# Kernel tuning notes

Hardware: AMD Instinct MI355X
Metric: run time of the kernel (lower is better)

Reference implementation:

```python
import jax, jax.numpy as jnp
import numpy as np

N_VERTICES = 24  # hardcoded via torch.eye(24) in the original
K = 3


def normalized_adj(adj):
    # scipy version: L = (A @ D^-1/2).T @ D^-1/2 = D^-1/2 @ A^T @ D^-1/2
    d = adj.sum(axis=1)
    d_inv_sqrt = jnp.where(d > 0, 1.0 / jnp.sqrt(d), 0.0)
    return (adj * d_inv_sqrt[None, :]).T * d_inv_sqrt[None, :]


def cheb_polynomials(L, k_order):
    Ts = [jnp.eye(N_VERTICES, dtype=L.dtype), L]
    for _ in range(2, k_order):
        Ts.append(2.0 * L @ Ts[-1] - Ts[-2])
    return jnp.stack(Ts[:k_order])  # (K, N, N)


def setup_inputs() -> dict:
    key = jax.random.key(0)
    k1, k2, k3 = jax.random.split(key, 3)
    x = jax.random.normal(k1, (64, 32, N_VERTICES, 512), dtype=jnp.float32)
    adj = jax.random.uniform(k2, (N_VERTICES, N_VERTICES), dtype=jnp.float32)
    Theta = jax.random.normal(k3, (K, 32, 32), dtype=jnp.float32)
    return {"x": x, "adj": adj, "Theta": Theta}


def reference(x, adj, Theta):
    # x: (b, c, n, t); adj: (n, n); Theta: (K, c, o)
    L = normalized_adj(adj)
    T = cheb_polynomials(L, K)  # (K, n, m)
    # original per-timestep, per-k: rhs[b,m,c] = sum_n x[b,n,c] T_k[n,m];
    # out[b,m,o] += rhs @ Theta_k. Fused over t and k, final permute -> (b,o,m,t).
    out = jnp.einsum('knm,bcnt,kco->bomt', T, x, Theta)
    return out
```

## Files before the change

### kernel.cpp

```cpp
#include <hip/hip_runtime.h>
#include <stdint.h>


#define NV 24
#define CIN 32
#define COUT 32
#define TDIM 512
#define BATCH 64
#define MDIM 768
#define KD 768
#define BM 128
#define BN 128
#define BK 32
#define NKT (KD / BK)
#define NTT (TDIM / BN)
#define NMT (MDIM / BM)
#define BLOB (BM * BK)

typedef __attribute__((ext_vector_type(8))) short short8v;
typedef __attribute__((ext_vector_type(4))) float float4v;

__device__ inline unsigned short f2bf(float f) {
    unsigned int u = __float_as_uint(f);
    unsigned int r = (u + 0x7fffu + ((u >> 16) & 1u)) >> 16;
    return (unsigned short)r;
}

__global__ __launch_bounds__(256) void prep_w(const float* __restrict__ adj,
                                              const float* __restrict__ Theta,
                                              unsigned short* __restrict__ Wp) {
    __shared__ float adjS[NV * NV];
    __shared__ float disS[NV];
    __shared__ float LS[NV * NV];
    __shared__ float T2S[NV * NV];
    int tid = threadIdx.x;
    for (int e = tid; e < NV * NV; e += 256) adjS[e] = adj[e];
    __syncthreads();
    if (tid < NV) {
        float d = 0.f;
        for (int j = 0; j < NV; ++j) d += adjS[tid * NV + j];
        disS[tid] = (d > 0.f) ? rsqrtf(d) : 0.f;
    }
    __syncthreads();
    for (int e = tid; e < NV * NV; e += 256) {
        int i = e / NV, j = e % NV;
        LS[e] = disS[i] * adjS[j * NV + i] * disS[j];
    }
    __syncthreads();
    for (int e = tid; e < NV * NV; e += 256) {
        int i = e / NV, j = e % NV;
        float s = 0.f;
        for (int p = 0; p < NV; ++p) s += LS[i * NV + p] * LS[p * NV + j];
        T2S[e] = 2.f * s - (i == j ? 1.f : 0.f);
    }
    __syncthreads();
    int r0 = blockIdx.x * (MDIM / 64);
    for (int e = tid; e < (MDIM / 64) * KD; e += 256) {
        int lr = e / KD, col = e % KD;
        int row = r0 + lr;
        int o = row / NV, m = row % NV;
        int c = col / NV, n = col % NV;
        float th0 = Theta[0 * CIN * COUT + c * COUT + o];
        float th1 = Theta[1 * CIN * COUT + c * COUT + o];
        float th2 = Theta[2 * CIN * COUT + c * COUT + o];
        float v = (n == m ? th0 : 0.f) + LS[n * NV + m] * th1 + T2S[n * NV + m] * th2;
        size_t idx = (((size_t)(row >> 7) * NKT + (col >> 5)) * BM + (row & 127)) * BK + (col & 31);
        Wp[idx] = f2bf(v);
    }
}

__global__ __launch_bounds__(256) void convert_xP(const float* __restrict__ x,
                                                  unsigned short* __restrict__ xP) {
    __shared__ float tile[BK][133];
    int kt = blockIdx.x % NKT;
    int tt = blockIdx.x / NKT;
    int b = blockIdx.y;
    int tid = threadIdx.x;
    const float* src = x + (size_t)b * KD * TDIM + (size_t)(kt * BK) * TDIM + tt * BN;
#pragma unroll
    for (int p = 0; p < 4; ++p) {
        int e = p * 256 + tid;
        int r = e >> 5, c4 = e & 31;
        float4 v = *(const float4*)(src + (size_t)r * TDIM + c4 * 4);
        tile[r][c4 * 4 + 0] = v.x;
        tile[r][c4 * 4 + 1] = v.y;
        tile[r][c4 * 4 + 2] = v.z;
        tile[r][c4 * 4 + 3] = v.w;
    }
    __syncthreads();
    unsigned short* dst = xP + ((size_t)(b * NTT + tt) * NKT + kt) * BLOB;
    int kq = tid & 7, tb = tid >> 3;
#pragma unroll
    for (int p = 0; p < 4; ++p) {
        int t = p * 32 + tb;
        ushort4 pk;
        pk.x = f2bf(tile[kq * 4 + 0][t]);
        pk.y = f2bf(tile[kq * 4 + 1][t]);
        pk.z = f2bf(tile[kq * 4 + 2][t]);
        pk.w = f2bf(tile[kq * 4 + 3][t]);
        *(ushort4*)(dst + t * BK + kq * 4) = pk;
    }
}

__global__ __launch_bounds__(256) void gemm_cheb(const unsigned short* __restrict__ Wp,
                                                 const unsigned short* __restrict__ xP,
                                                 float* __restrict__ out) {
    __shared__ __attribute__((aligned(16))) unsigned short As[BLOB];
    __shared__ __attribute__((aligned(16))) unsigned short Bs[BLOB];
    int b = blockIdx.y;
    int mt = blockIdx.x % NMT;
    int tt = blockIdx.x / NMT;
    int tid = threadIdx.x;
    int wave = tid >> 6;
    int lane = tid & 63;
    int quad = lane >> 4;
    int l16 = lane & 15;
    int wm = wave >> 1, wn = wave & 1;

    const unsigned short* Ab = Wp + (size_t)mt * NKT * BLOB;
    const unsigned short* Bb = xP + (size_t)(b * NTT + tt) * NKT * BLOB;

    const float4v zero4 = {0.f, 0.f, 0.f, 0.f};
    float4v acc[4][4];
#pragma unroll
    for (int i = 0; i < 4; ++i)
#pragma unroll
        for (int j = 0; j < 4; ++j) acc[i][j] = zero4;

    for (int kt = 0; kt < NKT; ++kt) {
        __syncthreads();
        const unsigned short* abase = Ab + (size_t)kt * BLOB;
        const unsigned short* bbase = Bb + (size_t)kt * BLOB;
#pragma unroll
        for (int h = 0; h < 2; ++h) {
            const unsigned short* sa = abase + (h * 256 + tid) * 8;
            const unsigned short* sb = bbase + (h * 256 + tid) * 8;
            unsigned short* da = As + (h * 256 + wave * 64) * 8;
            unsigned short* db = Bs + (h * 256 + wave * 64) * 8;
            __builtin_amdgcn_global_load_lds(
                (const __attribute__((address_space(1))) void*)sa,
                (__attribute__((address_space(3))) void*)da, 16, 0, 0);
            __builtin_amdgcn_global_load_lds(
                (const __attribute__((address_space(1))) void*)sb,
                (__attribute__((address_space(3))) void*)db, 16, 0, 0);
        }
        __syncthreads();
        short8v a[4], bb[4];
#pragma unroll
        for (int i = 0; i < 4; ++i)
            a[i] = *(const short8v*)(As + (wm * 64 + i * 16 + l16) * BK + quad * 8);
#pragma unroll
        for (int j = 0; j < 4; ++j)
            bb[j] = *(const short8v*)(Bs + (wn * 64 + j * 16 + l16) * BK + quad * 8);
#pragma unroll
        for (int i = 0; i < 4; ++i)
#pragma unroll
            for (int j = 0; j < 4; ++j)
                acc[i][j] = __builtin_amdgcn_mfma_f32_16x16x32_bf16(a[i], bb[j], acc[i][j], 0, 0, 0);
    }

    float* outB = out + (size_t)b * MDIM * TDIM;
    int rbase = mt * BM + wm * 64;
    int cbase = tt * BN + wn * 64;
#pragma unroll
    for (int i = 0; i < 4; ++i) {
#pragma unroll
        for (int j = 0; j < 4; ++j) {
            int row0 = rbase + i * 16 + quad * 4;
            int col = cbase + j * 16 + l16;
#pragma unroll
            for (int r = 0; r < 4; ++r)
                outB[(size_t)(row0 + r) * TDIM + col] = acc[i][j][r];
        }
    }
}

extern "C" void kernel_launch(void* const* d_in, const int* in_sizes, int n_in,
                              void* d_out, int out_size, void* d_ws, size_t ws_size,
                              hipStream_t stream) {
    const float* x = (const float*)d_in[0];
    const float* adj = (const float*)d_in[1];
    const float* Theta = (const float*)d_in[2];
    float* out = (float*)d_out;

    unsigned short* xP = (unsigned short*)d_ws;
    unsigned short* Wp = (unsigned short*)((char*)d_ws + (size_t)BATCH * TDIM * KD * 2);

    prep_w<<<64, 256, 0, stream>>>(adj, Theta, Wp);
    convert_xP<<<dim3(NKT * NTT, BATCH), 256, 0, stream>>>(x, xP);
    gemm_cheb<<<dim3(NMT * NTT, BATCH), 256, 0, stream>>>(Wp, xP, out);
}
```

Before: 245.3 us.

## Fuse x fp32-to-bf16 conversion into GEMM and remap blocks for L2 reuse

Drops the separate convert_xP kernel and its bf16 workspace round-trip. The GEMM now loads fp32 x tiles straight into LDS through an XOR-swizzled global_load_lds path and converts to bf16 while building the MFMA B fragments. The grid is also flattened and remapped so that groups of blocks sharing the same x tile run close together, improving L2 reuse across the six M tiles. In exchange, each block reads twice as many bytes of x and does the conversion work six times (once per M tile), and the strided scalar LDS reads may add bank conflicts.

```diff
diff --git a/kernel.cpp b/kernel.cpp
--- a/kernel.cpp
+++ b/kernel.cpp
@@ -1,4 +1,5 @@
 #include <hip/hip_runtime.h>
+#include <hip/hip_bf16.h>
 #include <stdint.h>
 
 
@@ -69,47 +70,20 @@
     }
 }
 
-__global__ __launch_bounds__(256) void convert_xP(const float* __restrict__ x,
-                                                  unsigned short* __restrict__ xP) {
-    __shared__ float tile[BK][133];
-    int kt = blockIdx.x % NKT;
-    int tt = blockIdx.x / NKT;
-    int b = blockIdx.y;
-    int tid = threadIdx.x;
-    const float* src = x + (size_t)b * KD * TDIM + (size_t)(kt * BK) * TDIM + tt * BN;
-#pragma unroll
-    for (int p = 0; p < 4; ++p) {
-        int e = p * 256 + tid;
-        int r = e >> 5, c4 = e & 31;
-        float4 v = *(const float4*)(src + (size_t)r * TDIM + c4 * 4);
-        tile[r][c4 * 4 + 0] = v.x;
-        tile[r][c4 * 4 + 1] = v.y;
-        tile[r][c4 * 4 + 2] = v.z;
-        tile[r][c4 * 4 + 3] = v.w;
-    }
-    __syncthreads();
-    unsigned short* dst = xP + ((size_t)(b * NTT + tt) * NKT + kt) * BLOB;
-    int kq = tid & 7, tb = tid >> 3;
-#pragma unroll
-    for (int p = 0; p < 4; ++p) {
-        int t = p * 32 + tb;
-        ushort4 pk;
-        pk.x = f2bf(tile[kq * 4 + 0][t]);
-        pk.y = f2bf(tile[kq * 4 + 1][t]);
-        pk.z = f2bf(tile[kq * 4 + 2][t]);
-        pk.w = f2bf(tile[kq * 4 + 3][t]);
-        *(ushort4*)(dst + t * BK + kq * 4) = pk;
-    }
-}
+__global__ __launch_bounds__(256) void gemm_fused(const unsigned short* __restrict__ Wp,
+                                                  const float* __restrict__ x,
+                                                  float* __restrict__ out) {
+    __shared__ __attribute__((aligned(16))) unsigned short As[BLOB];
+    __shared__ __attribute__((aligned(16))) float xF[BK * BN];
 
-__global__ __launch_bounds__(256) void gemm_cheb(const unsigned short* __restrict__ Wp,
-                                                 const unsigned short* __restrict__ xP,
-                                                 float* __restrict__ out) {
-    __shared__ __attribute__((aligned(16))) unsigned short As[BLOB];
-    __shared__ __attribute__((aligned(16))) unsigned short Bs[BLOB];
-    int b = blockIdx.y;
-    int mt = blockIdx.x % NMT;
-    int tt = blockIdx.x / NMT;
+    int id = blockIdx.x;
+    int hi = id / 48;
+    int rem = id - hi * 48;
+    int mt = rem >> 3;
+    int g = hi * 8 + (rem & 7);
+    int b = g >> 2;
+    int tt = g & 3;
+
     int tid = threadIdx.x;
     int wave = tid >> 6;
     int lane = tid & 63;
@@ -118,7 +92,7 @@
     int wm = wave >> 1, wn = wave & 1;
 
     const unsigned short* Ab = Wp + (size_t)mt * NKT * BLOB;
-    const unsigned short* Bb = xP + (size_t)(b * NTT + tt) * NKT * BLOB;
+    const float* xb = x + (size_t)b * KD * TDIM + tt * BN;
 
     const float4v zero4 = {0.f, 0.f, 0.f, 0.f};
     float4v acc[4][4];
@@ -130,28 +104,49 @@
     for (int kt = 0; kt < NKT; ++kt) {
         __syncthreads();
         const unsigned short* abase = Ab + (size_t)kt * BLOB;
-        const unsigned short* bbase = Bb + (size_t)kt * BLOB;
+        const float* xrow = xb + (size_t)(kt * BK) * TDIM;
 #pragma unroll
         for (int h = 0; h < 2; ++h) {
             const unsigned short* sa = abase + (h * 256 + tid) * 8;
-            const unsigned short* sb = bbase + (h * 256 + tid) * 8;
             unsigned short* da = As + (h * 256 + wave * 64) * 8;
-            unsigned short* db = Bs + (h * 256 + wave * 64) * 8;
             __builtin_amdgcn_global_load_lds(
                 (const __attribute__((address_space(1))) void*)sa,
                 (__attribute__((address_space(3))) void*)da, 16, 0, 0);
+        }
+#pragma unroll
+        for (int h = 0; h < 4; ++h) {
+            int lin = h * 256 + tid;
+            int k = lin >> 5;
+            int t4 = lin & 31;
+            int t4src = t4 ^ ((k >> 3) * 2);
+            const float* sx = xrow + (size_t)k * TDIM + t4src * 4;
+            float* dx = xF + (h * 1024 + wave * 256);
             __builtin_amdgcn_global_load_lds(
-                (const __attribute__((address_space(1))) void*)sb,
-                (__attribute__((address_space(3))) void*)db, 16, 0, 0);
+                (const __attribute__((address_space(1))) void*)sx,
+                (__attribute__((address_space(3))) void*)dx, 16, 0, 0);
         }
         __syncthreads();
-        short8v a[4], bb[4];
+
+        short8v a[4];
 #pragma unroll
         for (int i = 0; i < 4; ++i)
             a[i] = *(const short8v*)(As + (wm * 64 + i * 16 + l16) * BK + quad * 8);
+
+        short8v bb[4];
 #pragma unroll
-        for (int j = 0; j < 4; ++j)
-            bb[j] = *(const short8v*)(Bs + (wn * 64 + j * 16 + l16) * BK + quad * 8);
+        for (int j = 0; j < 4; ++j) {
+            int tloc = wn * 64 + j * 16 + l16;
+            int t4 = tloc >> 2, ti = tloc & 3;
+            const float* bp = xF + quad * 8 * BN + ((t4 ^ (quad * 2)) << 2) + ti;
+            float v0 = bp[0 * BN], v1 = bp[1 * BN], v2 = bp[2 * BN], v3 = bp[3 * BN];
+            float v4 = bp[4 * BN], v5 = bp[5 * BN], v6 = bp[6 * BN], v7 = bp[7 * BN];
+            union { short8v s; __hip_bfloat162 h[4]; } u;
+            u.h[0] = __float22bfloat162_rn({v0, v1});
+            u.h[1] = __float22bfloat162_rn({v2, v3});
+            u.h[2] = __float22bfloat162_rn({v4, v5});
+            u.h[3] = __float22bfloat162_rn({v6, v7});
+            bb[j] = u.s;
+        }
 #pragma unroll
         for (int i = 0; i < 4; ++i)
 #pragma unroll
@@ -183,10 +178,8 @@
     const float* Theta = (const float*)d_in[2];
     float* out = (float*)d_out;
 
-    unsigned short* xP = (unsigned short*)d_ws;
-    unsigned short* Wp = (unsigned short*)((char*)d_ws + (size_t)BATCH * TDIM * KD * 2);
+    unsigned short* Wp = (unsigned short*)d_ws;
 
     prep_w<<<64, 256, 0, stream>>>(adj, Theta, Wp);
-    convert_xP<<<dim3(NKT * NTT, BATCH), 256, 0, stream>>>(x, xP);
-    gemm_cheb<<<dim3(NMT * NTT, BATCH), 256, 0, stream>>>(Wp, xP, out);
+    gemm_fused<<<NMT * NTT * BATCH, 256, 0, stream>>>(Wp, x, out);
 }
```

Measured after the change: 236.7 us. 3.5% less time.
